# Optimization experiments

Measured on AMD Instinct MI355X. Metric: run time of the kernel, lower is better.

Reference implementation:

```python
import jax, jax.numpy as jnp
import numpy as np

EPS_LN = 1e-5
EPS_COS = 1e-8
EPS_AREA = 5e-4


def _ln(x, g, b):
    m = jnp.mean(x, axis=-1, keepdims=True)
    v = jnp.mean((x - m) ** 2, axis=-1, keepdims=True)
    return (x - m) / jnp.sqrt(v + EPS_LN) * g + b


def _wgap(f, m):
    # f: (b, N, c), m: (b, N) -> (b, c); matches masked avg_pool2d trick
    num = jnp.einsum('bnc,bn->bc', f, m)
    den = jnp.sum(m, axis=1, keepdims=True) + EPS_AREA
    return num / den


def _cos_tok(k, p):
    # k: (b, N, c) tokens vs p: (b, c) prototype, cosine over channel dim
    dot = jnp.einsum('bnc,bc->bn', k, p)
    nk = jnp.linalg.norm(k, axis=-1)
    np_ = jnp.linalg.norm(p, axis=-1, keepdims=True)
    return dot / (jnp.maximum(nk, EPS_COS) * jnp.maximum(np_, EPS_COS))


def _cos_vec(a, b):
    # a, b: (b, c) -> (b,)
    dot = jnp.sum(a * b, axis=-1)
    na = jnp.linalg.norm(a, axis=-1)
    nb = jnp.linalg.norm(b, axis=-1)
    return dot / (jnp.maximum(na, EPS_COS) * jnp.maximum(nb, EPS_COS))


def _mlp(x, W1, b1, W2, b2):
    h = jax.nn.gelu(x @ W1.T + b1, approximate=False)
    return h @ W2.T + b2


def setup_inputs() -> dict:
    key = jax.random.key(0)
    ks = jax.random.split(key, 32)
    b, H, W, c = 8, 64, 64, 512
    N = H * W
    hid = 4 * c
    s = 0.02
    inp = {
        'x': jax.random.normal(ks[0], (b, N, c), jnp.float32),
        'y': jax.random.normal(ks[1], (b, N, c), jnp.float32),
        'mask': (jax.random.uniform(ks[2], (b, N)) > 0.5).astype(jnp.float32),
        'pro_pred': jax.random.uniform(ks[3], (b, 1, H, W), jnp.float32),
        'g1': jnp.ones((c,), jnp.float32), 'beta1': jnp.zeros((c,), jnp.float32),
        'g2': jnp.ones((c,), jnp.float32), 'beta2': jnp.zeros((c,), jnp.float32),
        'Wq': jax.random.normal(ks[4], (c, c)) * s,
        'Wk': jax.random.normal(ks[5], (c, c)) * s,
        'Wv': jax.random.normal(ks[6], (c, c)) * s,
        'Wx1': jax.random.normal(ks[7], (c, 2 * c)) * s,
        'Wx2': jax.random.normal(ks[8], (c, 2 * c)) * s,
        'Wfx': jax.random.normal(ks[9], (c, 2 * c)) * s,
        'Wy1': jax.random.normal(ks[10], (c, 2 * c)) * s,
        'Wy2': jax.random.normal(ks[11], (c, 2 * c)) * s,
        'Wfy': jax.random.normal(ks[12], (c, 2 * c)) * s,
        'W1x': jax.random.normal(ks[13], (hid, c)) * s, 'b1x': jnp.zeros((hid,)),
        'W2x': jax.random.normal(ks[14], (c, hid)) * s, 'b2x': jnp.zeros((c,)),
        'W1y': jax.random.normal(ks[15], (hid, c)) * s, 'b1y': jnp.zeros((hid,)),
        'W2y': jax.random.normal(ks[16], (c, hid)) * s, 'b2y': jnp.zeros((c,)),
        'h': 64, 'w': 64,
    }
    return inp


def reference(x, y, mask, pro_pred, g1, beta1, g2, beta2, Wq, Wk, Wv,
              Wx1, Wx2, Wfx, Wy1, Wy2, Wfy,
              W1x, b1x, W2x, b2x, W1y, b1y, W2y, b2y, h, w):
    b, N, c = x.shape
    x_skip, y_skip = x, y
    xn = _ln(x, g1, beta1)
    yn = _ln(y, g1, beta1)
    q = yn @ Wq.T            # support features (b, N, c)
    k = xn @ Wk.T            # query features
    v = xn @ Wv.T

    m = mask                 # (b, N)
    fg_pro = _wgap(q, m)             # (b, c)
    bg_pro = _wgap(q, 1.0 - m)

    sim_fg = _cos_tok(k, fg_pro) * 10.0   # (b, N)
    sim_bg = _cos_tok(k, bg_pro) * 10.0
    logits = jnp.stack([sim_bg, sim_fg], axis=1)     # (b, 2, N)
    pseudo = jax.nn.softmax(logits, axis=1)

    query_fg1 = _wgap(v, pseudo[:, 1, :])            # (b, c)
    s1 = (_cos_vec(query_fg1, fg_pro)[:, None] + 1.0) / 2.0
    pro1 = s1 * fg_pro + (1.0 - s1) * query_fg1      # (b, c)

    query_fg2 = _wgap(v, pro_pred.reshape(b, N))
    s2 = (_cos_vec(query_fg2, fg_pro)[:, None] + 1.0) / 2.0
    pro2 = s2 * fg_pro + (1.0 - s2) * query_fg2

    p1 = jnp.broadcast_to(pro1[:, None, :], (b, N, c))
    p2 = jnp.broadcast_to(pro2[:, None, :], (b, N, c))

    x1 = jnp.concatenate([x_skip, p1], axis=-1) @ Wx1.T
    x2 = jnp.concatenate([x_skip, p2], axis=-1) @ Wx2.T
    x_merge = jnp.concatenate([x1, x2], axis=-1) @ Wfx.T + x_skip

    y1 = jnp.concatenate([y_skip, p1], axis=-1) @ Wy1.T
    y2 = jnp.concatenate([y_skip, p2], axis=-1) @ Wy2.T
    y_merge = jnp.concatenate([y1, y2], axis=-1) @ Wfy.T + y_skip

    x_out = x + _mlp(_ln(x_merge, g2, beta2), W1x, b1x, W2x, b2x)
    y_out = y + _mlp(_ln(y_merge, g2, beta2), W1y, b1y, W2y, b2y)
    pseudo_mask = pseudo.reshape(b, 2, h, w)
    return x_out, y_out, pseudo_mask
```

## Files before the change

### kernel.cpp

```cpp
#include <hip/hip_runtime.h>
#include <stdint.h>

typedef unsigned short u16;
typedef unsigned int   u32;

typedef __attribute__((ext_vector_type(8))) __bf16 bf16x8;
typedef __attribute__((ext_vector_type(4))) float  f32x4;

#define GLD_LDS(g, l) __builtin_amdgcn_global_load_lds( \
    (__attribute__((address_space(1))) void*)(g),        \
    (__attribute__((address_space(3))) void*)(l), 16, 0, 0)

__device__ __forceinline__ float bf2f(u16 h) {
    union { u32 u; float f; } c; c.u = ((u32)h) << 16; return c.f;
}
__device__ __forceinline__ u16 f2bf(float f) {
    union { float f; u32 u; } c; c.f = f;
    return (u16)((c.u + 0x7FFFu + ((c.u >> 16) & 1u)) >> 16);
}
__device__ __forceinline__ u32 pack2(float a, float b) {
    return (u32)f2bf(a) | ((u32)f2bf(b) << 16);
}
__device__ __forceinline__ uint4 pack8(float4 a, float4 b) {
    return make_uint4(pack2(a.x, a.y), pack2(a.z, a.w), pack2(b.x, b.y), pack2(b.z, b.w));
}
__device__ __forceinline__ void unpack8(uint4 u, float v[8]) {
    v[0] = bf2f((u16)(u.x & 0xffff)); v[1] = bf2f((u16)(u.x >> 16));
    v[2] = bf2f((u16)(u.y & 0xffff)); v[3] = bf2f((u16)(u.y >> 16));
    v[4] = bf2f((u16)(u.z & 0xffff)); v[5] = bf2f((u16)(u.z >> 16));
    v[6] = bf2f((u16)(u.w & 0xffff)); v[7] = bf2f((u16)(u.w >> 16));
}
__device__ __forceinline__ float wsum(float v) {
#pragma unroll
    for (int o = 32; o > 0; o >>= 1) v += __shfl_xor(v, o, 64);
    return v;
}

__global__ __launch_bounds__(256)
void cvt_kernel(const float* __restrict__ in, u16* __restrict__ out, int n8)
{
    const int i = blockIdx.x * 256 + threadIdx.x;
    if (i < n8) {
        const float* p = in + (size_t)i * 8;
        float4 a = *(const float4*)p, b = *(const float4*)(p + 4);
        *(uint4*)(out + (size_t)i * 8) = pack8(a, b);
    }
}

template<bool IN16, bool RAW>
__global__ __launch_bounds__(256)
void ln_kernel(const void* __restrict__ in, u16* __restrict__ out,
               const float* __restrict__ g, const float* __restrict__ be,
               u16* __restrict__ raw_out)
{
    const int lane = threadIdx.x & 63;
    const size_t row = (size_t)blockIdx.x * 4 + (threadIdx.x >> 6);
    const size_t base = row * 512 + lane * 8;
    float v[8];
    if constexpr (IN16) {
        unpack8(*(const uint4*)((const u16*)in + base), v);
    } else {
        const float* p = (const float*)in + base;
        float4 a = *(const float4*)p, b = *(const float4*)(p + 4);
        v[0]=a.x; v[1]=a.y; v[2]=a.z; v[3]=a.w; v[4]=b.x; v[5]=b.y; v[6]=b.z; v[7]=b.w;
    }
    if constexpr (RAW) {
        u32 ro[4];
#pragma unroll
        for (int i = 0; i < 4; ++i) ro[i] = pack2(v[2*i], v[2*i+1]);
        *(uint4*)(raw_out + base) = make_uint4(ro[0], ro[1], ro[2], ro[3]);
    }
    float s = 0.f, ss = 0.f;
#pragma unroll
    for (int i = 0; i < 8; ++i) { s += v[i]; ss += v[i] * v[i]; }
    s = wsum(s); ss = wsum(ss);
    const float mean = s * (1.f / 512.f);
    const float rstd = rsqrtf(ss * (1.f / 512.f) - mean * mean + 1e-5f);
    const float* gp = g + lane * 8;
    const float* bp = be + lane * 8;
    u32 o[4];
#pragma unroll
    for (int i = 0; i < 4; ++i) {
        u16 lo = f2bf((v[2*i]   - mean) * rstd * gp[2*i]   + bp[2*i]);
        u16 hi = f2bf((v[2*i+1] - mean) * rstd * gp[2*i+1] + bp[2*i+1]);
        o[i] = (u32)lo | ((u32)hi << 16);
    }
    *(uint4*)(out + base) = make_uint4(o[0], o[1], o[2], o[3]);
}

template<bool IS16>
__device__ __forceinline__ void load_pair(const void* P, size_t off, size_t rstep,
                                          uint4& r0, uint4& r1)
{
    if constexpr (IS16) {
        const u16* p = (const u16*)P + off;
        r0 = *(const uint4*)p;
        r1 = *(const uint4*)(p + rstep);
    } else {
        const float* p = (const float*)P + off;
        float4 a0 = *(const float4*)p,           a1 = *(const float4*)(p + 4);
        float4 b0 = *(const float4*)(p + rstep), b1 = *(const float4*)(p + rstep + 4);
        r0 = pack8(a0, a1);
        r1 = pack8(b0, b1);
    }
}

template<int EPI, bool OUT16>
__global__ __launch_bounds__(512)
void gemm3_kernel(const u16* __restrict__ A, const u16* __restrict__ B,
                  void* __restrict__ Cp, int N, int K,
                  const float* __restrict__ bias_b,
                  const float* __restrict__ bias_v,
                  const float* __restrict__ skip)
{
    __shared__ u16 sA[2][128 * 32];
    __shared__ u16 sB[2][256 * 32];
    const int t = threadIdx.x;
    const int w = t >> 6;
    const int lane = t & 63;
    const int lr = lane & 15;
    const int lk = lane >> 4;
    const int bm0 = blockIdx.x * 128;
    const int bn0 = blockIdx.y * 256;
    const int wrow = (w >> 2) * 64;
    const int wcol = (w & 3) * 64;

    f32x4 acc[4][4];
#pragma unroll
    for (int m = 0; m < 4; ++m)
#pragma unroll
        for (int n = 0; n < 4; ++n) acc[m][n] = (f32x4){0.f, 0.f, 0.f, 0.f};

    const int scol = ((t & 3) ^ ((t >> 3) & 3)) * 8;
    const u16* gA = A + (size_t)(bm0 + (t >> 2)) * K + scol;
    const u16* gB = B + (size_t)(bn0 + (t >> 2)) * K + scol;
    const size_t rstep = (size_t)128 * K;
    const int wo = w << 9;
    const int sa = (lk ^ ((lr >> 1) & 3)) * 8;

    GLD_LDS(gA, sA[0] + wo);
    GLD_LDS(gB, sB[0] + wo);
    GLD_LDS(gB + rstep, sB[0] + 4096 + wo);
    __syncthreads();

    int cur = 0;
    for (int kt = 32; kt <= K; kt += 32) {
        if (kt < K) {
            const int nxt = cur ^ 1;
            GLD_LDS(gA + kt, sA[nxt] + wo);
            GLD_LDS(gB + kt, sB[nxt] + wo);
            GLD_LDS(gB + kt + rstep, sB[nxt] + 4096 + wo);
        }
        bf16x8 af[4], bfr[4];
#pragma unroll
        for (int m = 0; m < 4; ++m)
            af[m] = *(const bf16x8*)&sA[cur][(wrow + m * 16 + lr) * 32 + sa];
#pragma unroll
        for (int n = 0; n < 4; ++n)
            bfr[n] = *(const bf16x8*)&sB[cur][(wcol + n * 16 + lr) * 32 + sa];
#pragma unroll
        for (int m = 0; m < 4; ++m)
#pragma unroll
            for (int n = 0; n < 4; ++n)
                acc[m][n] = __builtin_amdgcn_mfma_f32_16x16x32_bf16(af[m], bfr[n], acc[m][n], 0, 0, 0);
        if (kt < K) { __syncthreads(); cur ^= 1; }
    }

#pragma unroll
    for (int m = 0; m < 4; ++m) {
#pragma unroll
        for (int n = 0; n < 4; ++n) {
            const int col = bn0 + wcol + n * 16 + lr;
#pragma unroll
            for (int r = 0; r < 4; ++r) {
                const int row = bm0 + wrow + m * 16 + lk * 4 + r;
                const size_t idx = (size_t)row * N + col;
                float vv = acc[m][n][r];
                if (EPI == 1) vv += bias_b[(size_t)(row >> 12) * N + col] + skip[idx];
                if (EPI == 2) { vv += bias_v[col]; vv = 0.5f * vv * (1.f + erff(vv * 0.70710678118654752f)); }
                if (EPI == 3) vv += bias_v[col] + skip[idx];
                if (OUT16) ((u16*)Cp)[idx] = f2bf(vv);
                else       ((float*)Cp)[idx] = vv;
            }
        }
    }
}

template<int WM>
__global__ __launch_bounds__(512)
void gemm3_red_kernel(const u16* __restrict__ A, const u16* __restrict__ B, int K,
                      const float* __restrict__ wa, const float* __restrict__ wb,
                      float* __restrict__ acc1, float* __restrict__ acc2)
{
    __shared__ u16 sA[2][128 * 32];
    __shared__ u16 sB[2][256 * 32];
    __shared__ float sred[8][2][64];
    const int t = threadIdx.x;
    const int w = t >> 6;
    const int lane = t & 63;
    const int lr = lane & 15;
    const int lk = lane >> 4;
    const int bm0 = blockIdx.x * 128;
    const int bn0 = blockIdx.y * 256;
    const int wrow = (w >> 2) * 64;
    const int wcol = (w & 3) * 64;

    f32x4 acc[4][4];
#pragma unroll
    for (int m = 0; m < 4; ++m)
#pragma unroll
        for (int n = 0; n < 4; ++n) acc[m][n] = (f32x4){0.f, 0.f, 0.f, 0.f};

    const int scol = ((t & 3) ^ ((t >> 3) & 3)) * 8;
    const u16* gA = A + (size_t)(bm0 + (t >> 2)) * K + scol;
    const u16* gB = B + (size_t)(bn0 + (t >> 2)) * K + scol;
    const size_t rstep = (size_t)128 * K;
    const int wo = w << 9;
    const int sa = (lk ^ ((lr >> 1) & 3)) * 8;

    GLD_LDS(gA, sA[0] + wo);
    GLD_LDS(gB, sB[0] + wo);
    GLD_LDS(gB + rstep, sB[0] + 4096 + wo);
    __syncthreads();

    int cur = 0;
    for (int kt = 32; kt <= K; kt += 32) {
        if (kt < K) {
            const int nxt = cur ^ 1;
            GLD_LDS(gA + kt, sA[nxt] + wo);
            GLD_LDS(gB + kt, sB[nxt] + wo);
            GLD_LDS(gB + kt + rstep, sB[nxt] + 4096 + wo);
        }
        bf16x8 af[4], bfr[4];
#pragma unroll
        for (int m = 0; m < 4; ++m)
            af[m] = *(const bf16x8*)&sA[cur][(wrow + m * 16 + lr) * 32 + sa];
#pragma unroll
        for (int n = 0; n < 4; ++n)
            bfr[n] = *(const bf16x8*)&sB[cur][(wcol + n * 16 + lr) * 32 + sa];
#pragma unroll
        for (int m = 0; m < 4; ++m)
#pragma unroll
            for (int n = 0; n < 4; ++n)
                acc[m][n] = __builtin_amdgcn_mfma_f32_16x16x32_bf16(af[m], bfr[n], acc[m][n], 0, 0, 0);
        if (kt < K) { __syncthreads(); cur ^= 1; }
    }

    float w1v[16], w2v[16];
#pragma unroll
    for (int m = 0; m < 4; ++m)
#pragma unroll
        for (int r = 0; r < 4; ++r) {
            const int row = bm0 + wrow + m * 16 + lk * 4 + r;
            if (WM == 0) { float mm = wa[row]; w1v[m*4+r] = mm; w2v[m*4+r] = 1.f - mm; }
            else         { w1v[m*4+r] = wa[row]; w2v[m*4+r] = wb[row]; }
        }
    __syncthreads();
#pragma unroll
    for (int n = 0; n < 4; ++n) {
        float s1 = 0.f, s2 = 0.f;
#pragma unroll
        for (int m = 0; m < 4; ++m)
#pragma unroll
            for (int r = 0; r < 4; ++r) {
                s1 += acc[m][n][r] * w1v[m*4+r];
                s2 += acc[m][n][r] * w2v[m*4+r];
            }
        s1 += __shfl_xor(s1, 16, 64); s1 += __shfl_xor(s1, 32, 64);
        s2 += __shfl_xor(s2, 16, 64); s2 += __shfl_xor(s2, 32, 64);
        if (lk == 0) { sred[w][0][n*16+lr] = s1; sred[w][1][n*16+lr] = s2; }
    }
    __syncthreads();
    if (t < 256) {
        const int strip = t >> 6, c = t & 63;
        const float v1 = sred[strip][0][c] + sred[strip + 4][0][c];
        const float v2 = sred[strip][1][c] + sred[strip + 4][1][c];
        const int col = bn0 + strip * 64 + c;
        const int b = bm0 >> 12;
        atomicAdd(&acc1[b * 512 + col], v1);
        atomicAdd(&acc2[b * 512 + col], v2);
    }
}

template<int EPI, bool A16, bool B16, bool OUT16>
__global__ __launch_bounds__(256)
void gemm_kernel(const void* __restrict__ Ap, const void* __restrict__ Wp,
                 void* __restrict__ Cp, int N, int K,
                 const float* __restrict__ bias_b,
                 const float* __restrict__ bias_v,
                 const float* __restrict__ skip)
{
    __shared__ u16 sA[128 * 32];
    __shared__ u16 sB[128 * 32];
    const int t = threadIdx.x;
    const int w = t >> 6;
    const int lane = t & 63;
    const int lr = lane & 15;
    const int lk = lane >> 4;
    const int bm0 = blockIdx.x * 128;
    const int bn0 = blockIdx.y * 128;
    const int wrow = (w >> 1) * 64;
    const int wcol = (w & 1) * 64;

    f32x4 acc[4][4];
#pragma unroll
    for (int m = 0; m < 4; ++m)
#pragma unroll
        for (int n = 0; n < 4; ++n) acc[m][n] = (f32x4){0.f, 0.f, 0.f, 0.f};

    const size_t aoff = (size_t)(bm0 + (t >> 2)) * K + (t & 3) * 8;
    const size_t boff = (size_t)(bn0 + (t >> 2)) * K + (t & 3) * 8;
    const size_t rstep = (size_t)64 * K;
    u16* dA = sA + 8 * t;
    u16* dB = sB + 8 * t;

    for (int kt = 0; kt < K; kt += 32) {
        uint4 ra0, ra1, rb0, rb1;
        load_pair<A16>(Ap, aoff + kt, rstep, ra0, ra1);
        load_pair<B16>(Wp, boff + kt, rstep, rb0, rb1);
        __syncthreads();
        *(uint4*)dA = ra0; *(uint4*)(dA + 2048) = ra1;
        *(uint4*)dB = rb0; *(uint4*)(dB + 2048) = rb1;
        __syncthreads();
        bf16x8 af[4], bfr[4];
#pragma unroll
        for (int m = 0; m < 4; ++m)
            af[m] = *(const bf16x8*)&sA[(wrow + m * 16 + lr) * 32 + lk * 8];
#pragma unroll
        for (int n = 0; n < 4; ++n)
            bfr[n] = *(const bf16x8*)&sB[(wcol + n * 16 + lr) * 32 + lk * 8];
#pragma unroll
        for (int m = 0; m < 4; ++m)
#pragma unroll
            for (int n = 0; n < 4; ++n)
                acc[m][n] = __builtin_amdgcn_mfma_f32_16x16x32_bf16(af[m], bfr[n], acc[m][n], 0, 0, 0);
    }

#pragma unroll
    for (int m = 0; m < 4; ++m) {
#pragma unroll
        for (int n = 0; n < 4; ++n) {
            const int col = bn0 + wcol + n * 16 + lr;
#pragma unroll
            for (int r = 0; r < 4; ++r) {
                const int row = bm0 + wrow + m * 16 + lk * 4 + r;
                const size_t idx = (size_t)row * N + col;
                float vv = acc[m][n][r];
                if (EPI == 1) vv += bias_b[(size_t)(row >> 12) * N + col] + skip[idx];
                if (EPI == 2) { vv += bias_v[col]; vv = 0.5f * vv * (1.f + erff(vv * 0.70710678118654752f)); }
                if (EPI == 3) vv += bias_v[col] + skip[idx];
                if (OUT16) ((u16*)Cp)[idx] = f2bf(vv);
                else       ((float*)Cp)[idx] = vv;
            }
        }
    }
}

template<int WM>
__global__ __launch_bounds__(256)
void gemm_red_kernel(const u16* __restrict__ A, const float* __restrict__ W, int K,
                     const float* __restrict__ wa, const float* __restrict__ wb,
                     float* __restrict__ acc1, float* __restrict__ acc2)
{
    __shared__ u16 sA[128 * 32];
    __shared__ u16 sB[128 * 32];
    __shared__ float sred[4][2][64];
    const int t = threadIdx.x;
    const int w = t >> 6;
    const int lane = t & 63;
    const int lr = lane & 15;
    const int lk = lane >> 4;
    const int bm0 = blockIdx.x * 128;
    const int bn0 = blockIdx.y * 128;
    const int wrow = (w >> 1) * 64;
    const int wcol = (w & 1) * 64;

    f32x4 acc[4][4];
#pragma unroll
    for (int m = 0; m < 4; ++m)
#pragma unroll
        for (int n = 0; n < 4; ++n) acc[m][n] = (f32x4){0.f, 0.f, 0.f, 0.f};

    const size_t aoff = (size_t)(bm0 + (t >> 2)) * K + (t & 3) * 8;
    const size_t boff = (size_t)(bn0 + (t >> 2)) * K + (t & 3) * 8;
    const size_t rstep = (size_t)64 * K;
    u16* dA = sA + 8 * t;
    u16* dB = sB + 8 * t;

    for (int kt = 0; kt < K; kt += 32) {
        uint4 ra0, ra1, rb0, rb1;
        load_pair<true >(A, aoff + kt, rstep, ra0, ra1);
        load_pair<false>(W, boff + kt, rstep, rb0, rb1);
        __syncthreads();
        *(uint4*)dA = ra0; *(uint4*)(dA + 2048) = ra1;
        *(uint4*)dB = rb0; *(uint4*)(dB + 2048) = rb1;
        __syncthreads();
        bf16x8 af[4], bfr[4];
#pragma unroll
        for (int m = 0; m < 4; ++m)
            af[m] = *(const bf16x8*)&sA[(wrow + m * 16 + lr) * 32 + lk * 8];
#pragma unroll
        for (int n = 0; n < 4; ++n)
            bfr[n] = *(const bf16x8*)&sB[(wcol + n * 16 + lr) * 32 + lk * 8];
#pragma unroll
        for (int m = 0; m < 4; ++m)
#pragma unroll
            for (int n = 0; n < 4; ++n)
                acc[m][n] = __builtin_amdgcn_mfma_f32_16x16x32_bf16(af[m], bfr[n], acc[m][n], 0, 0, 0);
    }

    float w1v[16], w2v[16];
#pragma unroll
    for (int m = 0; m < 4; ++m)
#pragma unroll
        for (int r = 0; r < 4; ++r) {
            const int row = bm0 + wrow + m * 16 + lk * 4 + r;
            if (WM == 0) { float mm = wa[row]; w1v[m*4+r] = mm; w2v[m*4+r] = 1.f - mm; }
            else         { w1v[m*4+r] = wa[row]; w2v[m*4+r] = wb[row]; }
        }
#pragma unroll
    for (int n = 0; n < 4; ++n) {
        float s1 = 0.f, s2 = 0.f;
#pragma unroll
        for (int m = 0; m < 4; ++m)
#pragma unroll
            for (int r = 0; r < 4; ++r) {
                s1 += acc[m][n][r] * w1v[m*4+r];
                s2 += acc[m][n][r] * w2v[m*4+r];
            }
        s1 += __shfl_xor(s1, 16, 64); s1 += __shfl_xor(s1, 32, 64);
        s2 += __shfl_xor(s2, 16, 64); s2 += __shfl_xor(s2, 32, 64);
        if (lk == 0) { sred[w][0][n*16+lr] = s1; sred[w][1][n*16+lr] = s2; }
    }
    __syncthreads();
    if (t < 128) {
        const int half = t >> 6, c = t & 63;
        const float v1 = sred[half][0][c] + sred[half + 2][0][c];
        const float v2 = sred[half][1][c] + sred[half + 2][1][c];
        const int col = bn0 + half * 64 + c;
        const int b = bm0 >> 12;
        atomicAdd(&acc1[b * 512 + col], v1);
        atomicAdd(&acc2[b * 512 + col], v2);
    }
}

__global__ __launch_bounds__(256)
void rowsum_kernel(const float* __restrict__ in, float* __restrict__ out)
{
    __shared__ float sred[4];
    const int b = blockIdx.x, t = threadIdx.x;
    float s = 0.f;
    for (int i = 0; i < 16; ++i) s += in[b * 4096 + t + i * 256];
    s = wsum(s);
    if ((t & 63) == 0) sred[t >> 6] = s;
    __syncthreads();
    if (t == 0) out[b] = sred[0] + sred[1] + sred[2] + sred[3];
}

__global__ __launch_bounds__(512)
void proto_fin_kernel(const float* __restrict__ fgacc, const float* __restrict__ bgacc,
                      const float* __restrict__ denfg, float* __restrict__ fg_pro,
                      float* __restrict__ bg_pro, float* __restrict__ nfg, float* __restrict__ nbg)
{
    __shared__ float sred[16];
    const int b = blockIdx.x, c = threadIdx.x;
    const float d = denfg[b];
    const float fg = fgacc[b * 512 + c] / (d + 5e-4f);
    const float bg = bgacc[b * 512 + c] / ((4096.f - d) + 5e-4f);
    fg_pro[b * 512 + c] = fg; bg_pro[b * 512 + c] = bg;
    float s1 = wsum(fg * fg), s2 = wsum(bg * bg);
    if ((c & 63) == 0) { sred[c >> 6] = s1; sred[8 + (c >> 6)] = s2; }
    __syncthreads();
    if (c == 0) {
        float a = 0.f, bb = 0.f;
        for (int i = 0; i < 8; ++i) { a += sred[i]; bb += sred[8 + i]; }
        nfg[b] = sqrtf(a); nbg[b] = sqrtf(bb);
    }
}

__global__ __launch_bounds__(256)
void sim_kernel(const u16* __restrict__ k, const float* __restrict__ fg_pro,
                const float* __restrict__ bg_pro, const float* __restrict__ nfg,
                const float* __restrict__ nbg, float* __restrict__ pseudo_fg,
                float* __restrict__ pm)
{
    const int lane = threadIdx.x & 63;
    const int token = blockIdx.x * 4 + (threadIdx.x >> 6);
    const int b = token >> 12, n = token & 4095;
    uint4 u = *(const uint4*)(k + (size_t)token * 512 + lane * 8);
    float kv[8]; unpack8(u, kv);
    const float* fp = fg_pro + b * 512 + lane * 8;
    const float* bp = bg_pro + b * 512 + lane * 8;
    float dfg = 0.f, dbg = 0.f, kk = 0.f;
#pragma unroll
    for (int i = 0; i < 8; ++i) { dfg += kv[i] * fp[i]; dbg += kv[i] * bp[i]; kk += kv[i] * kv[i]; }
    dfg = wsum(dfg); dbg = wsum(dbg); kk = wsum(kk);
    const float nk = fmaxf(sqrtf(kk), 1e-8f);
    const float sfg = 10.f * dfg / (nk * fmaxf(nfg[b], 1e-8f));
    const float sbg = 10.f * dbg / (nk * fmaxf(nbg[b], 1e-8f));
    const float pfg = 1.f / (1.f + expf(sbg - sfg));
    if (lane == 0) {
        pseudo_fg[token] = pfg;
        pm[(size_t)b * 8192 + 4096 + n] = pfg;
        pm[(size_t)b * 8192 + n] = 1.f - pfg;
    }
}

__global__ __launch_bounds__(512)
void proto2_kernel(const float* __restrict__ q1acc, const float* __restrict__ q2acc,
                   const float* __restrict__ denq1, const float* __restrict__ denq2,
                   const float* __restrict__ fg_pro, const float* __restrict__ nfg,
                   float* __restrict__ pro1, float* __restrict__ pro2)
{
    __shared__ float sred[32];
    __shared__ float s1s, s2s;
    const int b = blockIdx.x, c = threadIdx.x;
    const float q1 = q1acc[b * 512 + c] / (denq1[b] + 5e-4f);
    const float q2 = q2acc[b * 512 + c] / (denq2[b] + 5e-4f);
    const float fg = fg_pro[b * 512 + c];
    float r0 = wsum(q1 * fg), r1 = wsum(q1 * q1), r2 = wsum(q2 * fg), r3 = wsum(q2 * q2);
    const int wv = c >> 6;
    if ((c & 63) == 0) { sred[wv] = r0; sred[8 + wv] = r1; sred[16 + wv] = r2; sred[24 + wv] = r3; }
    __syncthreads();
    if (c == 0) {
        float d1 = 0.f, n1 = 0.f, d2 = 0.f, n2 = 0.f;
        for (int i = 0; i < 8; ++i) { d1 += sred[i]; n1 += sred[8+i]; d2 += sred[16+i]; n2 += sred[24+i]; }
        const float nf = fmaxf(nfg[b], 1e-8f);
        s1s = (d1 / (fmaxf(sqrtf(n1), 1e-8f) * nf) + 1.f) * 0.5f;
        s2s = (d2 / (fmaxf(sqrtf(n2), 1e-8f) * nf) + 1.f) * 0.5f;
    }
    __syncthreads();
    pro1[b * 512 + c] = s1s * fg + (1.f - s1s) * q1;
    pro2[b * 512 + c] = s2s * fg + (1.f - s2s) * q2;
}

__global__ __launch_bounds__(256)
void mmcomb_kernel(const float* __restrict__ Wf, const float* __restrict__ W1,
                   const float* __restrict__ W2, u16* __restrict__ Mout)
{
    const int i = blockIdx.x * 16 + threadIdx.x;
    const int o = blockIdx.y * 16 + threadIdx.y;
    float s = 0.f;
    for (int j = 0; j < 512; ++j) {
        s += Wf[o * 1024 + j]       * W1[j * 1024 + i];
        s += Wf[o * 1024 + 512 + j] * W2[j * 1024 + i];
    }
    Mout[o * 512 + i] = f2bf(s);
}

__global__ __launch_bounds__(512)
void tvec_kernel(const float* __restrict__ W, const float* __restrict__ p, float* __restrict__ tout)
{
    const int lane = threadIdx.x & 63;
    const int j = blockIdx.x * 8 + (threadIdx.x >> 6);
    const int b = blockIdx.y;
    const float* wr = W + (size_t)j * 1024 + 512 + lane * 8;
    const float* pr = p + b * 512 + lane * 8;
    float4 w0 = *(const float4*)wr, w1 = *(const float4*)(wr + 4);
    float4 p0 = *(const float4*)pr, p1 = *(const float4*)(pr + 4);
    float s = w0.x*p0.x + w0.y*p0.y + w0.z*p0.z + w0.w*p0.w
            + w1.x*p1.x + w1.y*p1.y + w1.z*p1.z + w1.w*p1.w;
    s = wsum(s);
    if (lane == 0) tout[b * 512 + j] = s;
}

__global__ __launch_bounds__(512)
void biascomb_kernel(const float* __restrict__ Wf, const float* __restrict__ t1,
                     const float* __restrict__ t2, float* __restrict__ bias)
{
    const int lane = threadIdx.x & 63;
    const int o = blockIdx.x * 8 + (threadIdx.x >> 6);
    const int b = blockIdx.y;
    const float* w1 = Wf + (size_t)o * 1024 + lane * 8;
    const float* tp1 = t1 + b * 512 + lane * 8;
    const float* tp2 = t2 + b * 512 + lane * 8;
    float s = 0.f;
#pragma unroll
    for (int h = 0; h < 2; ++h) {
        const float* wv = w1 + h * 512;
        const float* tp = h ? tp2 : tp1;
        float4 a0 = *(const float4*)wv, a1 = *(const float4*)(wv + 4);
        float4 b0 = *(const float4*)tp, b1 = *(const float4*)(tp + 4);
        s += a0.x*b0.x + a0.y*b0.y + a0.z*b0.z + a0.w*b0.w
           + a1.x*b1.x + a1.y*b1.y + a1.z*b1.z + a1.w*b1.w;
    }
    s = wsum(s);
    if (lane == 0) bias[b * 512 + o] = s;
}

extern "C" void kernel_launch(void* const* d_in, const int* in_sizes, int n_in,
                              void* d_out, int out_size, void* d_ws, size_t ws_size,
                              hipStream_t stream)
{
    const float* x   = (const float*)d_in[0];
    const float* y   = (const float*)d_in[1];
    const float* mask= (const float*)d_in[2];
    const float* pp  = (const float*)d_in[3];
    const float* g1  = (const float*)d_in[4];
    const float* be1 = (const float*)d_in[5];
    const float* g2  = (const float*)d_in[6];
    const float* be2 = (const float*)d_in[7];
    const float* Wq  = (const float*)d_in[8];
    const float* Wk  = (const float*)d_in[9];
    const float* Wv  = (const float*)d_in[10];
    const float* Wx1 = (const float*)d_in[11];
    const float* Wx2 = (const float*)d_in[12];
    const float* Wfx = (const float*)d_in[13];
    const float* Wy1 = (const float*)d_in[14];
    const float* Wy2 = (const float*)d_in[15];
    const float* Wfy = (const float*)d_in[16];
    const float* W1x = (const float*)d_in[17];
    const float* b1x = (const float*)d_in[18];
    const float* W2x = (const float*)d_in[19];
    const float* b2x = (const float*)d_in[20];
    const float* W1y = (const float*)d_in[21];
    const float* b1y = (const float*)d_in[22];
    const float* W2y = (const float*)d_in[23];
    const float* b2y = (const float*)d_in[24];

    if (ws_size < 69206016u) return;
    const bool fast = ws_size >= 78643200u;
    const bool huge = ws_size >= 145752064u;

    float* outx = (float*)d_out;
    float* outy = outx + 16777216;
    float* pmf  = outx + 33554432;

    char* wsb = (char*)d_ws;
    float* fsm = (float*)wsb;
    float* fgacc  = fsm;
    float* bgacc  = fsm + 4096;
    float* q1acc  = fsm + 8192;
    float* q2acc  = fsm + 12288;
    float* denq1  = fsm + 16384;
    float* denfg  = fsm + 16392;
    float* denq2  = fsm + 16400;
    float* nfg    = fsm + 16408;
    float* nbg    = fsm + 16416;
    float* fg_pro = fsm + 16424;
    float* bg_pro = fsm + 20520;
    float* pro1   = fsm + 24616;
    float* pro2   = fsm + 28712;
    float* t1x    = fsm + 32808;
    float* t2x    = fsm + 36904;
    float* t1y    = fsm + 41000;
    float* t2y    = fsm + 45096;
    float* bias_x = fsm + 49192;
    float* bias_y = fsm + 53288;
    float* pseudo = fsm + 57384;

    hipMemsetAsync(fsm, 0, 65568, stream);

    if (fast) {
        u16* Mx   = (u16*)(wsb + 0x60000);
        u16* My   = (u16*)(wsb + 0xE0000);
        u16* Wqb  = (u16*)(wsb + 0x160000);
        u16* Wkb  = (u16*)(wsb + 0x1E0000);
        u16* Wvb  = (u16*)(wsb + 0x260000);
        u16* W1xb = (u16*)(wsb + 0x2E0000);
        u16* W2xb = (u16*)(wsb + 0x4E0000);
        u16* W1yb = (u16*)(wsb + 0x6E0000);
        u16* W2yb = (u16*)(wsb + 0x8E0000);
        u16* WS0  = (u16*)(wsb + 0xB00000);
        u16* WS1  = WS0 + 16777216;
        u16* WS2  = WS1 + 16777216;

        u16* OX0 = (u16*)outx;
        u16* OX1 = OX0 + 16777216;
        u16* OY  = (u16*)outy;

        cvt_kernel<<<128, 256, 0, stream>>>(Wq,  Wqb,  32768);
        cvt_kernel<<<128, 256, 0, stream>>>(Wk,  Wkb,  32768);
        cvt_kernel<<<128, 256, 0, stream>>>(Wv,  Wvb,  32768);
        cvt_kernel<<<512, 256, 0, stream>>>(W1x, W1xb, 131072);
        cvt_kernel<<<512, 256, 0, stream>>>(W2x, W2xb, 131072);
        cvt_kernel<<<512, 256, 0, stream>>>(W1y, W1yb, 131072);
        cvt_kernel<<<512, 256, 0, stream>>>(W2y, W2yb, 131072);
        mmcomb_kernel<<<dim3(32, 32), dim3(16, 16), 0, stream>>>(Wfx, Wx1, Wx2, Mx);
        mmcomb_kernel<<<dim3(32, 32), dim3(16, 16), 0, stream>>>(Wfy, Wy1, Wy2, My);

        ln_kernel<false, true><<<8192, 256, 0, stream>>>(x, WS0, g1, be1, OX0);
        ln_kernel<false, true><<<8192, 256, 0, stream>>>(y, WS1, g1, be1, OY);

        dim3 gq(256, 2);
        gemm3_red_kernel<0><<<gq, 512, 0, stream>>>(WS1, Wqb, 512, mask, nullptr, fgacc, bgacc);
        rowsum_kernel<<<8, 256, 0, stream>>>(mask, denfg);
        rowsum_kernel<<<8, 256, 0, stream>>>(pp, denq2);
        proto_fin_kernel<<<8, 512, 0, stream>>>(fgacc, bgacc, denfg, fg_pro, bg_pro, nfg, nbg);

        gemm3_kernel<0, true><<<gq, 512, 0, stream>>>(WS0, Wkb, OX1, 512, 512, nullptr, nullptr, nullptr);
        sim_kernel<<<8192, 256, 0, stream>>>(OX1, fg_pro, bg_pro, nfg, nbg, pseudo, pmf);
        rowsum_kernel<<<8, 256, 0, stream>>>(pseudo, denq1);

        gemm3_red_kernel<1><<<gq, 512, 0, stream>>>(WS0, Wvb, 512, pseudo, pp, q1acc, q2acc);
        proto2_kernel<<<8, 512, 0, stream>>>(q1acc, q2acc, denq1, denq2, fg_pro, nfg, pro1, pro2);

        dim3 gtv(64, 8);
        tvec_kernel<<<gtv, 512, 0, stream>>>(Wx1, pro1, t1x);
        tvec_kernel<<<gtv, 512, 0, stream>>>(Wx2, pro2, t2x);
        tvec_kernel<<<gtv, 512, 0, stream>>>(Wy1, pro1, t1y);
        tvec_kernel<<<gtv, 512, 0, stream>>>(Wy2, pro2, t2y);
        biascomb_kernel<<<gtv, 512, 0, stream>>>(Wfx, t1x, t2x, bias_x);
        biascomb_kernel<<<gtv, 512, 0, stream>>>(Wfy, t1y, t2y, bias_y);

        gemm3_kernel<1, true><<<gq, 512, 0, stream>>>(OX0, Mx, WS0, 512, 512, bias_x, nullptr, x);
        ln_kernel<true, false><<<8192, 256, 0, stream>>>(WS0, WS1, g2, be2, nullptr);
        gemm3_kernel<1, true><<<gq, 512, 0, stream>>>(OY, My, WS0, 512, 512, bias_y, nullptr, y);
        ln_kernel<true, false><<<8192, 256, 0, stream>>>(WS0, WS0, g2, be2, nullptr);

        for (int ch = 0; ch < 2; ++ch) {
            const size_t ro = (size_t)ch * 16384 * 512;
            gemm3_kernel<2, true><<<dim3(128, 8), 512, 0, stream>>>(WS1 + ro, W1xb, OY, 2048, 512, nullptr, b1x, nullptr);
            gemm3_kernel<3, false><<<dim3(128, 2), 512, 0, stream>>>(OY, W2xb, outx + ro, 512, 2048, nullptr, b2x, x + ro);
        }

        if (huge) {
            for (int ch = 0; ch < 2; ++ch) {
                const size_t ro = (size_t)ch * 16384 * 512;
                gemm3_kernel<2, true><<<dim3(128, 8), 512, 0, stream>>>(WS0 + ro, W1yb, WS2, 2048, 512, nullptr, b1y, nullptr);
                gemm3_kernel<3, false><<<dim3(128, 2), 512, 0, stream>>>(WS2, W2yb, outy + ro, 512, 2048, nullptr, b2y, y + ro);
            }
        } else {
            for (int ch = 0; ch < 4; ++ch) {
                const size_t ro = (size_t)ch * 8192 * 512;
                gemm3_kernel<2, true><<<dim3(64, 8), 512, 0, stream>>>(WS0 + ro, W1yb, WS1, 2048, 512, nullptr, b1y, nullptr);
                gemm3_kernel<3, false><<<dim3(64, 2), 512, 0, stream>>>(WS1, W2yb, outy + ro, 512, 2048, nullptr, b2y, y + ro);
            }
        }
    } else {
        u16* Mx  = (u16*)(wsb + 360608);
        u16* My  = (u16*)(wsb + 884896);
        u16* WS0 = (u16*)(wsb + 2097152);
        u16* WS1 = (u16*)(wsb + 35651584);

        ln_kernel<false, false><<<8192, 256, 0, stream>>>(x, WS0, g1, be1, nullptr);
        ln_kernel<false, false><<<8192, 256, 0, stream>>>(y, WS1, g1, be1, nullptr);

        dim3 g512(256, 4);
        gemm_red_kernel<0><<<g512, 256, 0, stream>>>(WS1, Wq, 512, mask, nullptr, fgacc, bgacc);
        rowsum_kernel<<<8, 256, 0, stream>>>(mask, denfg);
        rowsum_kernel<<<8, 256, 0, stream>>>(pp, denq2);
        proto_fin_kernel<<<8, 512, 0, stream>>>(fgacc, bgacc, denfg, fg_pro, bg_pro, nfg, nbg);

        gemm_kernel<0, true, false, true><<<g512, 256, 0, stream>>>(WS0, Wk, WS1, 512, 512, nullptr, nullptr, nullptr);
        sim_kernel<<<8192, 256, 0, stream>>>(WS1, fg_pro, bg_pro, nfg, nbg, pseudo, pmf);
        rowsum_kernel<<<8, 256, 0, stream>>>(pseudo, denq1);

        gemm_red_kernel<1><<<g512, 256, 0, stream>>>(WS0, Wv, 512, pseudo, pp, q1acc, q2acc);
        proto2_kernel<<<8, 512, 0, stream>>>(q1acc, q2acc, denq1, denq2, fg_pro, nfg, pro1, pro2);

        mmcomb_kernel<<<dim3(32, 32), dim3(16, 16), 0, stream>>>(Wfx, Wx1, Wx2, Mx);
        mmcomb_kernel<<<dim3(32, 32), dim3(16, 16), 0, stream>>>(Wfy, Wy1, Wy2, My);
        dim3 gtv(64, 8);
        tvec_kernel<<<gtv, 512, 0, stream>>>(Wx1, pro1, t1x);
        tvec_kernel<<<gtv, 512, 0, stream>>>(Wx2, pro2, t2x);
        tvec_kernel<<<gtv, 512, 0, stream>>>(Wy1, pro1, t1y);
        tvec_kernel<<<gtv, 512, 0, stream>>>(Wy2, pro2, t2y);
        biascomb_kernel<<<gtv, 512, 0, stream>>>(Wfx, t1x, t2x, bias_x);
        biascomb_kernel<<<gtv, 512, 0, stream>>>(Wfy, t1y, t2y, bias_y);

        gemm_kernel<1, false, true, true><<<g512, 256, 0, stream>>>(x, Mx, WS0, 512, 512, bias_x, nullptr, x);
        ln_kernel<true, false><<<8192, 256, 0, stream>>>(WS0, WS1, g2, be2, nullptr);
        for (int ch = 0; ch < 4; ++ch) {
            const size_t ro = (size_t)ch * 8192 * 512;
            gemm_kernel<2, true, false, true><<<dim3(64, 16), 256, 0, stream>>>(WS1 + ro, W1x, WS0, 2048, 512, nullptr, b1x, nullptr);
            gemm_kernel<3, true, false, false><<<dim3(64, 4), 256, 0, stream>>>(WS0, W2x, outx + ro, 512, 2048, nullptr, b2x, x + ro);
        }
        gemm_kernel<1, false, true, true><<<g512, 256, 0, stream>>>(y, My, WS0, 512, 512, bias_y, nullptr, y);
        ln_kernel<true, false><<<8192, 256, 0, stream>>>(WS0, WS1, g2, be2, nullptr);
        for (int ch = 0; ch < 4; ++ch) {
            const size_t ro = (size_t)ch * 8192 * 512;
            gemm_kernel<2, true, false, true><<<dim3(64, 16), 256, 0, stream>>>(WS1 + ro, W1y, WS0, 2048, 512, nullptr, b1y, nullptr);
            gemm_kernel<3, true, false, false><<<dim3(64, 4), 256, 0, stream>>>(WS0, W2y, outy + ro, 512, 2048, nullptr, b2y, y + ro);
        }
    }
    (void)in_sizes; (void)n_in; (void)out_size;
}
```

Baseline: 926.2 us.

## Use tanh-approx GELU and smaller-tile GEMM for MLP down-projection

Replaces the exact erf-based GELU in the GEMM epilogues with a sigmoid/exp form of the tanh approximation. It also adds a 128x128-tile, 256-thread GEMM variant and uses it for the second MLP matmul (N=512, K=2048), doubling the number of blocks over the previous 128x256 tiles. The goal is cheaper epilogue math and better occupancy and load balance for the narrow-N GEMM. The GELU change alters numerics relative to the exact-erf reference, though the error is small.

After: 903.6 us. 2.4% less time.

```diff
diff --git a/kernel.cpp b/kernel.cpp
--- a/kernel.cpp
+++ b/kernel.cpp
@@ -34,6 +34,10 @@
 #pragma unroll
     for (int o = 32; o > 0; o >>= 1) v += __shfl_xor(v, o, 64);
     return v;
+}
+__device__ __forceinline__ float fast_gelu(float x) {
+    const float u = x * (1.f + 0.044715f * x * x);
+    return x / (1.f + __expf(-1.5957691216f * u));
 }
 
 __global__ __launch_bounds__(256)
@@ -177,7 +181,86 @@
                 const size_t idx = (size_t)row * N + col;
                 float vv = acc[m][n][r];
                 if (EPI == 1) vv += bias_b[(size_t)(row >> 12) * N + col] + skip[idx];
-                if (EPI == 2) { vv += bias_v[col]; vv = 0.5f * vv * (1.f + erff(vv * 0.70710678118654752f)); }
+                if (EPI == 2) { vv += bias_v[col]; vv = fast_gelu(vv); }
+                if (EPI == 3) vv += bias_v[col] + skip[idx];
+                if (OUT16) ((u16*)Cp)[idx] = f2bf(vv);
+                else       ((float*)Cp)[idx] = vv;
+            }
+        }
+    }
+}
+
+template<int EPI, bool OUT16>
+__global__ __launch_bounds__(256)
+void gemm2_kernel(const u16* __restrict__ A, const u16* __restrict__ B,
+                  void* __restrict__ Cp, int N, int K,
+                  const float* __restrict__ bias_b,
+                  const float* __restrict__ bias_v,
+                  const float* __restrict__ skip)
+{
+    __shared__ u16 sA[2][128 * 32];
+    __shared__ u16 sB[2][128 * 32];
+    const int t = threadIdx.x;
+    const int w = t >> 6;
+    const int lane = t & 63;
+    const int lr = lane & 15;
+    const int lk = lane >> 4;
+    const int bm0 = blockIdx.x * 128;
+    const int bn0 = blockIdx.y * 128;
+    const int wrow = (w >> 1) * 64;
+    const int wcol = (w & 1) * 64;
+
+    f32x4 acc[4][4];
+#pragma unroll
+    for (int m = 0; m < 4; ++m)
+#pragma unroll
+        for (int n = 0; n < 4; ++n) acc[m][n] = (f32x4){0.f, 0.f, 0.f, 0.f};
+
+    const int scol = ((t & 3) ^ ((t >> 3) & 3)) * 8;
+    const u16* gA = A + (size_t)(bm0 + (t >> 2)) * K + scol;
+    const u16* gB = B + (size_t)(bn0 + (t >> 2)) * K + scol;
+    const size_t rstep = (size_t)64 * K;
+    const int wo = w << 9;
+    const int sa = (lk ^ ((lr >> 1) & 3)) * 8;
+
+    GLD_LDS(gA, sA[0] + wo); GLD_LDS(gA + rstep, sA[0] + wo + 2048);
+    GLD_LDS(gB, sB[0] + wo); GLD_LDS(gB + rstep, sB[0] + wo + 2048);
+    __syncthreads();
+
+    int cur = 0;
+    for (int kt = 32; kt <= K; kt += 32) {
+        if (kt < K) {
+            const int nxt = cur ^ 1;
+            GLD_LDS(gA + kt, sA[nxt] + wo); GLD_LDS(gA + kt + rstep, sA[nxt] + wo + 2048);
+            GLD_LDS(gB + kt, sB[nxt] + wo); GLD_LDS(gB + kt + rstep, sB[nxt] + wo + 2048);
+        }
+        bf16x8 af[4], bfr[4];
+#pragma unroll
+        for (int m = 0; m < 4; ++m)
+            af[m] = *(const bf16x8*)&sA[cur][(wrow + m * 16 + lr) * 32 + sa];
+#pragma unroll
+        for (int n = 0; n < 4; ++n)
+            bfr[n] = *(const bf16x8*)&sB[cur][(wcol + n * 16 + lr) * 32 + sa];
+#pragma unroll
+        for (int m = 0; m < 4; ++m)
+#pragma unroll
+            for (int n = 0; n < 4; ++n)
+                acc[m][n] = __builtin_amdgcn_mfma_f32_16x16x32_bf16(af[m], bfr[n], acc[m][n], 0, 0, 0);
+        if (kt < K) { __syncthreads(); cur ^= 1; }
+    }
+
+#pragma unroll
+    for (int m = 0; m < 4; ++m) {
+#pragma unroll
+        for (int n = 0; n < 4; ++n) {
+            const int col = bn0 + wcol + n * 16 + lr;
+#pragma unroll
+            for (int r = 0; r < 4; ++r) {
+                const int row = bm0 + wrow + m * 16 + lk * 4 + r;
+                const size_t idx = (size_t)row * N + col;
+                float vv = acc[m][n][r];
+                if (EPI == 1) vv += bias_b[(size_t)(row >> 12) * N + col] + skip[idx];
+                if (EPI == 2) { vv += bias_v[col]; vv = fast_gelu(vv); }
                 if (EPI == 3) vv += bias_v[col] + skip[idx];
                 if (OUT16) ((u16*)Cp)[idx] = f2bf(vv);
                 else       ((float*)Cp)[idx] = vv;
@@ -347,7 +430,7 @@
                 const size_t idx = (size_t)row * N + col;
                 float vv = acc[m][n][r];
                 if (EPI == 1) vv += bias_b[(size_t)(row >> 12) * N + col] + skip[idx];
-                if (EPI == 2) { vv += bias_v[col]; vv = 0.5f * vv * (1.f + erff(vv * 0.70710678118654752f)); }
+                if (EPI == 2) { vv += bias_v[col]; vv = fast_gelu(vv); }
                 if (EPI == 3) vv += bias_v[col] + skip[idx];
                 if (OUT16) ((u16*)Cp)[idx] = f2bf(vv);
                 else       ((float*)Cp)[idx] = vv;
@@ -711,20 +794,20 @@
         for (int ch = 0; ch < 2; ++ch) {
             const size_t ro = (size_t)ch * 16384 * 512;
             gemm3_kernel<2, true><<<dim3(128, 8), 512, 0, stream>>>(WS1 + ro, W1xb, OY, 2048, 512, nullptr, b1x, nullptr);
-            gemm3_kernel<3, false><<<dim3(128, 2), 512, 0, stream>>>(OY, W2xb, outx + ro, 512, 2048, nullptr, b2x, x + ro);
+            gemm2_kernel<3, false><<<dim3(128, 4), 256, 0, stream>>>(OY, W2xb, outx + ro, 512, 2048, nullptr, b2x, x + ro);
         }
 
         if (huge) {
             for (int ch = 0; ch < 2; ++ch) {
                 const size_t ro = (size_t)ch * 16384 * 512;
                 gemm3_kernel<2, true><<<dim3(128, 8), 512, 0, stream>>>(WS0 + ro, W1yb, WS2, 2048, 512, nullptr, b1y, nullptr);
-                gemm3_kernel<3, false><<<dim3(128, 2), 512, 0, stream>>>(WS2, W2yb, outy + ro, 512, 2048, nullptr, b2y, y + ro);
+                gemm2_kernel<3, false><<<dim3(128, 4), 256, 0, stream>>>(WS2, W2yb, outy + ro, 512, 2048, nullptr, b2y, y + ro);
             }
         } else {
             for (int ch = 0; ch < 4; ++ch) {
                 const size_t ro = (size_t)ch * 8192 * 512;
                 gemm3_kernel<2, true><<<dim3(64, 8), 512, 0, stream>>>(WS0 + ro, W1yb, WS1, 2048, 512, nullptr, b1y, nullptr);
-                gemm3_kernel<3, false><<<dim3(64, 2), 512, 0, stream>>>(WS1, W2yb, outy + ro, 512, 2048, nullptr, b2y, y + ro);
+                gemm2_kernel<3, false><<<dim3(64, 4), 256, 0, stream>>>(WS1, W2yb, outy + ro, 512, 2048, nullptr, b2y, y + ro);
             }
         }
     } else {
```
